# Kernel tuning notes

Measured on AMD Instinct MI355X. Metric: run time of the kernel, lower is better.

The kernel has to match this reference:

```python
import jax, jax.numpy as jnp
import numpy as np

B, L, C = 4, 2048, 1024

def setup_inputs() -> dict:
    key = jax.random.key(0)
    k1, k2, k3 = jax.random.split(key, 3)
    net_in = jax.random.normal(k1, (B, L, C), dtype=jnp.float32)
    # torch Linear weights stored as (out, in); we keep that convention
    w_qkv = jax.random.normal(k2, (3 * C, C), dtype=jnp.float32) * (1.0 / np.sqrt(C))
    w_out = jax.random.normal(k3, (C, C), dtype=jnp.float32) * (1.0 / np.sqrt(C))
    return {"net_in": net_in, "w_qkv": w_qkv, "w_out": w_out}

def reference(net_in, w_qkv, w_out):
    Bc, Lc, Cc = net_in.shape
    qkv = jnp.einsum('blc,dc->bld', net_in, w_qkv)  # (B, L, 3C)
    q, k, v = jnp.split(qkv, 3, axis=-1)
    attn = jnp.einsum('bqc,bkc->bqk', q, k) / jnp.sqrt(jnp.float32(Cc))
    causal = jnp.tril(jnp.ones((Lc, Lc), dtype=bool))
    attn = jnp.where(causal[None, :, :], attn, -jnp.inf)
    attn = jax.nn.softmax(attn, axis=-1)
    out = jnp.einsum('bqk,bkc->bqc', attn, v)
    return jnp.einsum('blc,dc->bld', out, w_out)
```

## Files before the change

kernel.cpp:

```cpp
#include <hip/hip_runtime.h>
#include <hip/hip_bf16.h>
#include <cstdint>
#include <cstddef>

typedef __hip_bfloat16 bf16;
typedef float  floatx4 __attribute__((ext_vector_type(4)));
typedef __bf16 bf16x8  __attribute__((ext_vector_type(8)));

typedef __attribute__((address_space(1))) void as1_void;
typedef __attribute__((address_space(3))) void as3_void;

constexpr int Bn = 4, Ln = 2048, Cn = 1024;

__device__ __forceinline__ void store_one(float* p, float v) { *p = v; }
__device__ __forceinline__ void store_one(bf16*  p, float v) { *p = __float2bfloat16(v); }

#define BAR()    asm volatile("s_barrier" ::: "memory")
#define VMCNT0() asm volatile("s_waitcnt vmcnt(0)" ::: "memory")
#define SCHEDB() __builtin_amdgcn_sched_barrier(0)
#define STAGE(gp, off) \
    __builtin_amdgcn_global_load_lds((const as1_void*)(gp), (as3_void*)(smem + (off)), 16, 0, 0)

template <typename OutT>
__device__ __forceinline__ void gemm128(
    char* __restrict__ smem,
    const bf16* __restrict__ A, const bf16* __restrict__ B, OutT* __restrict__ C,
    int m0, int n0, int kend, int lda, int ldb, int ldc, float cscale)
{
    const int tid  = threadIdx.x;
    const int lane = tid & 63;
    const int quad = lane >> 4;
    const int lr   = lane & 15;
    const int wave = tid >> 6;
    const int wm   = (wave >> 2) * 64;
    const int wn   = (wave & 3) * 32;

    floatx4 acc[4][2];
#pragma unroll
    for (int i = 0; i < 4; ++i)
#pragma unroll
        for (int j = 0; j < 2; ++j) { floatx4 z = {0.f, 0.f, 0.f, 0.f}; acc[i][j] = z; }

    const int srow = tid >> 3;
    const int sx   = (tid & 7) ^ (srow & 7);
    const bf16* gA = A + (size_t)(m0 + srow) * lda + sx * 8;
    const bf16* gB = B + (size_t)(n0 + srow) * ldb + sx * 8;
    const int wuni = __builtin_amdgcn_readfirstlane((tid & 0x1C0) * 16);

    const int aoff = (wm + lr) * 64;
    const int boff = (wn + lr) * 64;
    const int s0   = (quad ^ (lr & 7)) * 8;

    const int NT  = kend >> 6;
    const int BUF = 32768;

#define STG4(KN, bo) do { \
        STAGE(gA + (KN),            (bo) + 0 * 8192 + wuni); \
        STAGE(gA + (KN) + 64 * lda, (bo) + 1 * 8192 + wuni); \
        STAGE(gB + (KN),            (bo) + 16384 + 0 * 8192 + wuni); \
        STAGE(gB + (KN) + 64 * ldb, (bo) + 16384 + 1 * 8192 + wuni); } while (0)

    STG4(0, 0);
    VMCNT0();
    BAR();

#define LDA2(PH, SK) do { _Pragma("unroll") for (int ii = 0; ii < 2; ++ii) \
        a[ii] = *(const bf16x8*)(As + aoff + ((PH) * 2 + ii) * 1024 + (SK)); } while (0)
#define LDB2(SK) do { _Pragma("unroll") for (int nn = 0; nn < 2; ++nn) \
        b[nn] = *(const bf16x8*)(Bs + boff + nn * 1024 + (SK)); } while (0)
#define MFMA4(PH) do { _Pragma("unroll") for (int ii = 0; ii < 2; ++ii) { \
        _Pragma("unroll") for (int nn = 0; nn < 2; ++nn) \
            acc[(PH) * 2 + ii][nn] = __builtin_amdgcn_mfma_f32_16x16x32_bf16( \
                a[ii], b[nn], acc[(PH) * 2 + ii][nn], 0, 0, 0); } } while (0)

    for (int t = 0; t < NT; ++t) {
        const bf16* As = (const bf16*)(smem + (t & 1) * BUF);
        const bf16* Bs = (const bf16*)(smem + (t & 1) * BUF + 16384);
        const int  wl  = ((t + 1) & 1) * BUF;
        const int  kn  = (t + 1) << 6;
        const bool more = (t + 1 < NT);
        bf16x8 a[2], b[2];

        LDB2(s0);
        LDA2(0, s0);
        if (more) STG4(kn, wl);
        BAR(); SCHEDB();
        __builtin_amdgcn_s_setprio(1);
        MFMA4(0);
        __builtin_amdgcn_s_setprio(0);
        SCHEDB();
        BAR();

        LDA2(1, s0);
        BAR(); SCHEDB();
        __builtin_amdgcn_s_setprio(1);
        MFMA4(1);
        __builtin_amdgcn_s_setprio(0);
        SCHEDB();
        BAR();

        LDB2(s0 ^ 32);
        LDA2(0, s0 ^ 32);
        BAR(); SCHEDB();
        __builtin_amdgcn_s_setprio(1);
        MFMA4(0);
        __builtin_amdgcn_s_setprio(0);
        SCHEDB();
        BAR();

        LDA2(1, s0 ^ 32);
        BAR(); SCHEDB();
        __builtin_amdgcn_s_setprio(1);
        MFMA4(1);
        __builtin_amdgcn_s_setprio(0);
        SCHEDB();
        if (more) VMCNT0();
        BAR();
    }
#undef LDA2
#undef LDB2
#undef MFMA4
#undef STG4

#pragma unroll
    for (int mi = 0; mi < 4; ++mi) {
        const int row = m0 + wm + mi * 16 + quad * 4;
#pragma unroll
        for (int n = 0; n < 2; ++n) {
            const int col = n0 + wn + n * 16 + lr;
            OutT* cp = C + (size_t)row * ldc + col;
#pragma unroll
            for (int r = 0; r < 4; ++r)
                store_one(cp + (size_t)r * ldc, acc[mi][n][r] * cscale);
        }
    }
}

__global__ __launch_bounds__(512, 4)
void g1_qk(const bf16* __restrict__ Xb, const bf16* __restrict__ Wqkb,
           bf16* __restrict__ QK)
{
    __shared__ __align__(16) char smem[65536];
    const int i = blockIdx.x;
    const int x = i & 7;
    const int r = i >> 3;
    const int mt = x * 8 + (r & 7);
    const int nt = r >> 3;
    gemm128<bf16>(smem, Xb, Wqkb, QK, mt * 128, nt * 128, 1024, 1024, 1024, 2048, 1.0f);
}

__global__ __launch_bounds__(512, 4)
void g2_s_w2(const bf16* __restrict__ QK, const bf16* __restrict__ Wob,
             const bf16* __restrict__ WvT, bf16* __restrict__ S,
             bf16* __restrict__ W2)
{
    __shared__ __align__(16) char smem[65536];
    const int i = blockIdx.x;
    if (i < 544) {
        const int b = (i & 7) >> 1;
        const int p = i & 1;
        const int t = (i >> 3) * 2 + p;
        int ti = (int)((sqrtf(8.f * t + 1.f) - 1.f) * 0.5f);
        while ((ti + 1) * (ti + 2) / 2 <= t) ++ti;
        while (ti * (ti + 1) / 2 > t) --ti;
        const int tj = t - ti * (ti + 1) / 2;
        const bf16* Aq = QK + (size_t)b * Ln * 2048;
        const bf16* Bk = Aq + 1024;
        bf16* Sb = S + (size_t)b * Ln * Ln;
        gemm128<bf16>(smem, Aq, Bk, Sb, ti * 128, tj * 128, 1024, 2048, 2048, Ln, 0.03125f);
    } else {
        const int j = i - 544;
        gemm128<bf16>(smem, Wob, WvT, W2, (j >> 3) * 128, (j & 7) * 128, 1024, 1024, 1024, 1024, 1.0f);
    }
}

__device__ __forceinline__ float waveMax(float x) {
#pragma unroll
    for (int o = 32; o > 0; o >>= 1) x = fmaxf(x, __shfl_xor(x, o, 64));
    return x;
}
__device__ __forceinline__ float waveSum(float x) {
#pragma unroll
    for (int o = 32; o > 0; o >>= 1) x += __shfl_xor(x, o, 64);
    return x;
}

__device__ void softmax_rows16(bf16* __restrict__ S, int i)
{
    const int wave = threadIdx.x >> 6, lane = threadIdx.x & 63;
    for (int it2 = 0; it2 < 2; ++it2) {
        const int row = i + 512 * (wave * 2 + it2);
        const int q = row & (Ln - 1);
        bf16* Srow = S + (size_t)row * Ln;
        const int kmax = ((q >> 7) + 1) << 7;
        const int nv = (kmax + 511) >> 9;
        float x[4][8];
        float m = -1e30f;
        for (int it = 0; it < nv; ++it) {
            int c0 = it * 512 + lane * 8;
            bf16x8 v = *(const bf16x8*)(Srow + c0);
#pragma unroll
            for (int e = 0; e < 8; ++e) {
                float f = (float)v[e];
                f = (c0 + e <= q) ? f : -1e30f;
                x[it][e] = f;
                m = fmaxf(m, f);
            }
        }
        m = waveMax(m);
        float s = 0.f;
        for (int it = 0; it < nv; ++it)
#pragma unroll
            for (int e = 0; e < 8; ++e) {
                float ex = (x[it][e] > -1e29f) ? __expf(x[it][e] - m) : 0.f;
                x[it][e] = ex;
                s += ex;
            }
        s = waveSum(s);
        const float inv = 1.f / s;
        for (int it = 0; it < nv; ++it) {
            bf16x8 o;
#pragma unroll
            for (int e = 0; e < 8; ++e) o[e] = (__bf16)(x[it][e] * inv);
            *(bf16x8*)(Srow + it * 512 + lane * 8) = o;
        }
    }
}

__global__ __launch_bounds__(512, 4)
void g3_vwt_sm(const bf16* __restrict__ W2, const bf16* __restrict__ Xb,
               bf16* __restrict__ VWT, bf16* __restrict__ S)
{
    __shared__ __align__(16) char smem[65536];
    const int i = blockIdx.x;
    const int x = i & 7;
    const int r = i >> 3;
    const int nt = x * 8 + (r & 7);
    const int mh = r >> 3;
    gemm128<bf16>(smem, W2, Xb, VWT, mh * 128, nt * 128, 1024, 1024, 1024, 8192, 1.0f);
    softmax_rows16(S, i);
}

__global__ __launch_bounds__(512, 4)
void g4_out(const bf16* __restrict__ P, const bf16* __restrict__ VWT,
            float* __restrict__ out)
{
    __shared__ __align__(16) char smem[65536];
    const int i = blockIdx.x;
    const int b = (i & 7) >> 1, p = i & 1;
    const int nt = p * 4 + ((i >> 3) & 3);
    const int mh = 15 - (i >> 5);

    const bf16* Pp = P + (size_t)b * Ln * Ln;
    const bf16* Bv = VWT + (size_t)b * Ln;
    float* Co = out + (size_t)b * Ln * Cn;
    gemm128<float>(smem, Pp, Bv, Co, mh * 128, nt * 128, (mh + 1) * 128, Ln, 8192, Cn, 1.0f);
}

__global__ __launch_bounds__(256)
void cast_all(const float* __restrict__ X, const float* __restrict__ Wqkv,
              const float* __restrict__ Wo,
              bf16* __restrict__ Xb, bf16* __restrict__ Wqkb,
              bf16* __restrict__ Wob, bf16* __restrict__ WvT)
{
    int blk = blockIdx.x;
    if (blk < 11264) {
        int i = blk * 256 + threadIdx.x;
        const float* src; bf16* dst; int off;
        if (i < 2097152)                 { src = X;    dst = Xb;   off = i; }
        else if (i < 2097152 + 524288)   { src = Wqkv; dst = Wqkb; off = i - 2097152; }
        else                             { src = Wo;   dst = Wob;  off = i - 2621440; }
        float4 f = ((const float4*)src)[off];
        bf16 o0 = __float2bfloat16(f.x), o1 = __float2bfloat16(f.y);
        bf16 o2 = __float2bfloat16(f.z), o3 = __float2bfloat16(f.w);
        ushort4 u;
        u.x = *(unsigned short*)&o0; u.y = *(unsigned short*)&o1;
        u.z = *(unsigned short*)&o2; u.w = *(unsigned short*)&o3;
        *(ushort4*)(dst + (size_t)off * 4) = u;
    } else {
        __shared__ float t[32][33];
        int tt = blk - 11264;
        int c0 = (tt & 31) * 32;
        int r0 = (tt >> 5) * 32;
        const float* Wv = Wqkv + 2048 * 1024;
        int xcol = threadIdx.x & 31, y0 = threadIdx.x >> 5;
#pragma unroll
        for (int p = 0; p < 4; ++p) {
            int y = y0 + 8 * p;
            t[y][xcol] = Wv[(size_t)(r0 + y) * 1024 + c0 + xcol];
        }
        __syncthreads();
#pragma unroll
        for (int p = 0; p < 4; ++p) {
            int mloc = y0 + 8 * p;
            WvT[(size_t)(c0 + mloc) * 1024 + r0 + xcol] = __float2bfloat16(t[xcol][mloc]);
        }
    }
}

extern "C" void kernel_launch(void* const* d_in, const int* in_sizes, int n_in,
                              void* d_out, int out_size, void* d_ws, size_t ws_size,
                              hipStream_t stream)
{
    const float* X    = (const float*)d_in[0];
    const float* Wqkv = (const float*)d_in[1];
    const float* Wout = (const float*)d_in[2];
    float* out = (float*)d_out;

    char* ws = (char*)d_ws;
    const size_t MiB = 1024ull * 1024ull;
    bf16* Xb   = (bf16*)(ws + 0);
    bf16* QK   = (bf16*)(ws + 16 * MiB);
    bf16* VWT  = (bf16*)(ws + 48 * MiB);
    bf16* Sbuf = (bf16*)(ws + 64 * MiB);
    bf16* Wqkb = (bf16*)(ws + 96 * MiB);
    bf16* WvT  = (bf16*)(ws + 100 * MiB);
    bf16* Wob  = (bf16*)(ws + 102 * MiB);
    bf16* W2   = (bf16*)(ws + 104 * MiB);

    cast_all<<<dim3(12288), 256, 0, stream>>>(X, Wqkv, Wout, Xb, Wqkb, Wob, WvT);

    g1_qk<<<dim3(1024), 512, 0, stream>>>(Xb, Wqkb, QK);

    g2_s_w2<<<dim3(608), 512, 0, stream>>>(QK, Wob, WvT, Sbuf, W2);

    g3_vwt_sm<<<dim3(512), 512, 0, stream>>>(W2, Xb, VWT, Sbuf);

    g4_out<<<dim3(512), 512, 0, stream>>>(Sbuf, VWT, out);
}
```

Baseline: 228.2 us.

## Use 128x256 single-buffered GEMM tiles and rebalance work across kernels

Adds a 128x256 tile GEMM with a single 48KB LDS buffer and uses it for the QK projection, the Wout·Wv product and the VWT GEMM. The W2 GEMM moves from the S kernel into the QK kernel, and softmax runs in its own blocks instead of after each GEMM block in g3. Larger tiles raise arithmetic intensity and cut block count. In exchange, the single-buffered loop waits on every K-tile load with no overlap, and register pressure rises with a 4x4 accumulator array.

```diff
diff --git a/kernel.cpp b/kernel.cpp
--- a/kernel.cpp
+++ b/kernel.cpp
@@ -20,6 +20,88 @@
 #define SCHEDB() __builtin_amdgcn_sched_barrier(0)
 #define STAGE(gp, off) \
     __builtin_amdgcn_global_load_lds((const as1_void*)(gp), (as3_void*)(smem + (off)), 16, 0, 0)
+
+template <typename OutT>
+__device__ __forceinline__ void gemm_sb_m128n256(
+    char* __restrict__ smem,
+    const bf16* __restrict__ A, const bf16* __restrict__ B, OutT* __restrict__ C,
+    int m0, int n0, int kend, int lda, int ldb, int ldc, float cscale)
+{
+    const int tid  = threadIdx.x;
+    const int lane = tid & 63;
+    const int quad = lane >> 4;
+    const int lr   = lane & 15;
+    const int wave = tid >> 6;
+    const int wm   = (wave >> 2) * 64;
+    const int wn   = (wave & 3) * 64;
+
+    floatx4 acc[4][4];
+#pragma unroll
+    for (int i = 0; i < 4; ++i)
+#pragma unroll
+        for (int j = 0; j < 4; ++j) { floatx4 z = {0.f, 0.f, 0.f, 0.f}; acc[i][j] = z; }
+
+    const int srow = tid >> 3;
+    const int sx   = (tid & 7) ^ (srow & 7);
+    const bf16* gA = A + (size_t)(m0 + srow) * lda + sx * 8;
+    const bf16* gB = B + (size_t)(n0 + srow) * ldb + sx * 8;
+    const int wuni = __builtin_amdgcn_readfirstlane((tid & 0x1C0) * 16);
+
+    const int aoff = (wm + lr) * 64;
+    const int boff = (wn + lr) * 64;
+    const int s0   = (quad ^ (lr & 7)) * 8;
+
+    const int NT = kend >> 6;
+    const bf16* As = (const bf16*)smem;
+    const bf16* Bs = (const bf16*)(smem + 16384);
+
+    for (int t = 0; t < NT; ++t) {
+        const int kn = t << 6;
+        STAGE(gA + kn,             0 * 8192 + wuni);
+        STAGE(gA + kn + 64 * lda,  1 * 8192 + wuni);
+        STAGE(gB + kn,             16384 + 0 * 8192 + wuni);
+        STAGE(gB + kn + 64  * ldb, 16384 + 1 * 8192 + wuni);
+        STAGE(gB + kn + 128 * ldb, 16384 + 2 * 8192 + wuni);
+        STAGE(gB + kn + 192 * ldb, 16384 + 3 * 8192 + wuni);
+        VMCNT0();
+        BAR();
+        SCHEDB();
+#pragma unroll
+        for (int kk = 0; kk < 2; ++kk) {
+            const int sk = s0 ^ (kk << 5);
+            bf16x8 a[4], b[4];
+#pragma unroll
+            for (int ii = 0; ii < 4; ++ii)
+                a[ii] = *(const bf16x8*)(As + aoff + ii * 1024 + sk);
+#pragma unroll
+            for (int nn = 0; nn < 4; ++nn)
+                b[nn] = *(const bf16x8*)(Bs + boff + nn * 1024 + sk);
+            __builtin_amdgcn_s_setprio(1);
+#pragma unroll
+            for (int ii = 0; ii < 4; ++ii)
+#pragma unroll
+                for (int nn = 0; nn < 4; ++nn)
+                    acc[ii][nn] = __builtin_amdgcn_mfma_f32_16x16x32_bf16(
+                        a[ii], b[nn], acc[ii][nn], 0, 0, 0);
+            __builtin_amdgcn_s_setprio(0);
+        }
+        SCHEDB();
+        if (t + 1 < NT) BAR();
+    }
+
+#pragma unroll
+    for (int mi = 0; mi < 4; ++mi) {
+        const int row = m0 + wm + mi * 16 + quad * 4;
+#pragma unroll
+        for (int n = 0; n < 4; ++n) {
+            const int col = n0 + wn + n * 16 + lr;
+            OutT* cp = C + (size_t)row * ldc + col;
+#pragma unroll
+            for (int r = 0; r < 4; ++r)
+                store_one(cp + (size_t)r * ldc, acc[mi][n][r] * cscale);
+        }
+    }
+}
 
 template <typename OutT>
 __device__ __forceinline__ void gemm128(
@@ -138,40 +220,39 @@
 
 __global__ __launch_bounds__(512, 4)
 void g1_qk(const bf16* __restrict__ Xb, const bf16* __restrict__ Wqkb,
-           bf16* __restrict__ QK)
+           const bf16* __restrict__ Wob, const bf16* __restrict__ WvT,
+           bf16* __restrict__ QK, bf16* __restrict__ W2)
+{
+    __shared__ __align__(16) char smem[49152];
+    const int i = blockIdx.x;
+    if (i < 512) {
+        const int x = i & 7;
+        const int r = i >> 3;
+        const int mt = x * 8 + (r & 7);
+        const int nt = r >> 3;
+        gemm_sb_m128n256<bf16>(smem, Xb, Wqkb, QK, mt * 128, nt * 256, 1024, 1024, 1024, 2048, 1.0f);
+    } else {
+        const int j = i - 512;
+        gemm_sb_m128n256<bf16>(smem, Wob, WvT, W2, (j >> 2) * 128, (j & 3) * 256, 1024, 1024, 1024, 1024, 1.0f);
+    }
+}
+
+__global__ __launch_bounds__(512, 4)
+void g2_s(const bf16* __restrict__ QK, bf16* __restrict__ S)
 {
     __shared__ __align__(16) char smem[65536];
     const int i = blockIdx.x;
-    const int x = i & 7;
-    const int r = i >> 3;
-    const int mt = x * 8 + (r & 7);
-    const int nt = r >> 3;
-    gemm128<bf16>(smem, Xb, Wqkb, QK, mt * 128, nt * 128, 1024, 1024, 1024, 2048, 1.0f);
-}
-
-__global__ __launch_bounds__(512, 4)
-void g2_s_w2(const bf16* __restrict__ QK, const bf16* __restrict__ Wob,
-             const bf16* __restrict__ WvT, bf16* __restrict__ S,
-             bf16* __restrict__ W2)
-{
-    __shared__ __align__(16) char smem[65536];
-    const int i = blockIdx.x;
-    if (i < 544) {
-        const int b = (i & 7) >> 1;
-        const int p = i & 1;
-        const int t = (i >> 3) * 2 + p;
-        int ti = (int)((sqrtf(8.f * t + 1.f) - 1.f) * 0.5f);
-        while ((ti + 1) * (ti + 2) / 2 <= t) ++ti;
-        while (ti * (ti + 1) / 2 > t) --ti;
-        const int tj = t - ti * (ti + 1) / 2;
-        const bf16* Aq = QK + (size_t)b * Ln * 2048;
-        const bf16* Bk = Aq + 1024;
-        bf16* Sb = S + (size_t)b * Ln * Ln;
-        gemm128<bf16>(smem, Aq, Bk, Sb, ti * 128, tj * 128, 1024, 2048, 2048, Ln, 0.03125f);
-    } else {
-        const int j = i - 544;
-        gemm128<bf16>(smem, Wob, WvT, W2, (j >> 3) * 128, (j & 7) * 128, 1024, 1024, 1024, 1024, 1.0f);
-    }
+    const int b = (i & 7) >> 1;
+    const int p = i & 1;
+    const int t = (i >> 3) * 2 + p;
+    int ti = (int)((sqrtf(8.f * t + 1.f) - 1.f) * 0.5f);
+    while ((ti + 1) * (ti + 2) / 2 <= t) ++ti;
+    while (ti * (ti + 1) / 2 > t) --ti;
+    const int tj = t - ti * (ti + 1) / 2;
+    const bf16* Aq = QK + (size_t)b * Ln * 2048;
+    const bf16* Bk = Aq + 1024;
+    bf16* Sb = S + (size_t)b * Ln * Ln;
+    gemm128<bf16>(smem, Aq, Bk, Sb, ti * 128, tj * 128, 1024, 2048, 2048, Ln, 0.03125f);
 }
 
 __device__ __forceinline__ float waveMax(float x) {
@@ -185,11 +266,11 @@
     return x;
 }
 
-__device__ void softmax_rows16(bf16* __restrict__ S, int i)
+__device__ void softmax_rows32(bf16* __restrict__ S, int idx)
 {
     const int wave = threadIdx.x >> 6, lane = threadIdx.x & 63;
-    for (int it2 = 0; it2 < 2; ++it2) {
-        const int row = i + 512 * (wave * 2 + it2);
+    for (int it4 = 0; it4 < 4; ++it4) {
+        const int row = idx + 256 * (wave * 4 + it4);
         const int q = row & (Ln - 1);
         bf16* Srow = S + (size_t)row * Ln;
         const int kmax = ((q >> 7) + 1) << 7;
@@ -231,14 +312,17 @@
 void g3_vwt_sm(const bf16* __restrict__ W2, const bf16* __restrict__ Xb,
                bf16* __restrict__ VWT, bf16* __restrict__ S)
 {
-    __shared__ __align__(16) char smem[65536];
+    __shared__ __align__(16) char smem[49152];
     const int i = blockIdx.x;
-    const int x = i & 7;
-    const int r = i >> 3;
-    const int nt = x * 8 + (r & 7);
-    const int mh = r >> 3;
-    gemm128<bf16>(smem, W2, Xb, VWT, mh * 128, nt * 128, 1024, 1024, 1024, 8192, 1.0f);
-    softmax_rows16(S, i);
+    if (i < 256) {
+        const int x = i & 7;
+        const int r = i >> 3;
+        const int nt = x * 4 + (r & 3);
+        const int mh = r >> 2;
+        gemm_sb_m128n256<bf16>(smem, W2, Xb, VWT, mh * 128, nt * 256, 1024, 1024, 1024, 8192, 1.0f);
+    } else {
+        softmax_rows32(S, i - 256);
+    }
 }
 
 __global__ __launch_bounds__(512, 4)
@@ -320,9 +404,9 @@
 
     cast_all<<<dim3(12288), 256, 0, stream>>>(X, Wqkv, Wout, Xb, Wqkb, Wob, WvT);
 
-    g1_qk<<<dim3(1024), 512, 0, stream>>>(Xb, Wqkb, QK);
-
-    g2_s_w2<<<dim3(608), 512, 0, stream>>>(QK, Wob, WvT, Sbuf, W2);
+    g1_qk<<<dim3(544), 512, 0, stream>>>(Xb, Wqkb, Wob, WvT, QK, W2);
+
+    g2_s<<<dim3(544), 512, 0, stream>>>(QK, Sbuf);
 
     g3_vwt_sm<<<dim3(512), 512, 0, stream>>>(W2, Xb, VWT, Sbuf);
 
```

After: 233.4 us. 1.02x slower.

## Rebalance stages: move W2 into QK kernel, VWT into S kernel, standalone softmax, paired out tiles

Applied to the files above, without the earlier changes.

The W2 = Wo·WvT GEMM now runs in the first kernel alongside the QK projection, and the VWT GEMM runs alongside the causal S GEMM, so each launch has more independent work. Softmax becomes its own kernel with 256 blocks handling four rows per wave. The output GEMM pairs a long and a short causal row tile in each block (h and 15-h), giving every block equal work across half as many blocks. The aim is to even out the triangular load imbalance and cut tail effects between stages, at the cost of one extra launch and softmax no longer overlapping with a GEMM.

```diff
diff --git a/kernel.cpp b/kernel.cpp
--- a/kernel.cpp
+++ b/kernel.cpp
@@ -138,21 +138,27 @@
 
 __global__ __launch_bounds__(512, 4)
 void g1_qk(const bf16* __restrict__ Xb, const bf16* __restrict__ Wqkb,
-           bf16* __restrict__ QK)
+           const bf16* __restrict__ Wob, const bf16* __restrict__ WvT,
+           bf16* __restrict__ QK, bf16* __restrict__ W2)
 {
     __shared__ __align__(16) char smem[65536];
     const int i = blockIdx.x;
-    const int x = i & 7;
-    const int r = i >> 3;
-    const int mt = x * 8 + (r & 7);
-    const int nt = r >> 3;
-    gemm128<bf16>(smem, Xb, Wqkb, QK, mt * 128, nt * 128, 1024, 1024, 1024, 2048, 1.0f);
+    if (i < 1024) {
+        const int x = i & 7;
+        const int r = i >> 3;
+        const int mt = x * 8 + (r & 7);
+        const int nt = r >> 3;
+        gemm128<bf16>(smem, Xb, Wqkb, QK, mt * 128, nt * 128, 1024, 1024, 1024, 2048, 1.0f);
+    } else {
+        const int j = i - 1024;
+        gemm128<bf16>(smem, Wob, WvT, W2, (j >> 3) * 128, (j & 7) * 128, 1024, 1024, 1024, 1024, 1.0f);
+    }
 }
 
 __global__ __launch_bounds__(512, 4)
-void g2_s_w2(const bf16* __restrict__ QK, const bf16* __restrict__ Wob,
-             const bf16* __restrict__ WvT, bf16* __restrict__ S,
-             bf16* __restrict__ W2)
+void g2_sv(const bf16* __restrict__ QK, const bf16* __restrict__ W2,
+           const bf16* __restrict__ Xb, bf16* __restrict__ S,
+           bf16* __restrict__ VWT)
 {
     __shared__ __align__(16) char smem[65536];
     const int i = blockIdx.x;
@@ -170,7 +176,11 @@
         gemm128<bf16>(smem, Aq, Bk, Sb, ti * 128, tj * 128, 1024, 2048, 2048, Ln, 0.03125f);
     } else {
         const int j = i - 544;
-        gemm128<bf16>(smem, Wob, WvT, W2, (j >> 3) * 128, (j & 7) * 128, 1024, 1024, 1024, 1024, 1.0f);
+        const int x = j & 7;
+        const int r = j >> 3;
+        const int nt = x * 8 + (r & 7);
+        const int mh = r >> 3;
+        gemm128<bf16>(smem, W2, Xb, VWT, mh * 128, nt * 128, 1024, 1024, 1024, 8192, 1.0f);
     }
 }
 
@@ -185,11 +195,13 @@
     return x;
 }
 
-__device__ void softmax_rows16(bf16* __restrict__ S, int i)
-{
+__global__ __launch_bounds__(512)
+void g3_sm(bf16* __restrict__ S)
+{
+    const int idx = blockIdx.x;
     const int wave = threadIdx.x >> 6, lane = threadIdx.x & 63;
-    for (int it2 = 0; it2 < 2; ++it2) {
-        const int row = i + 512 * (wave * 2 + it2);
+    for (int it4 = 0; it4 < 4; ++it4) {
+        const int row = idx + 256 * (wave * 4 + it4);
         const int q = row & (Ln - 1);
         bf16* Srow = S + (size_t)row * Ln;
         const int kmax = ((q >> 7) + 1) << 7;
@@ -228,20 +240,6 @@
 }
 
 __global__ __launch_bounds__(512, 4)
-void g3_vwt_sm(const bf16* __restrict__ W2, const bf16* __restrict__ Xb,
-               bf16* __restrict__ VWT, bf16* __restrict__ S)
-{
-    __shared__ __align__(16) char smem[65536];
-    const int i = blockIdx.x;
-    const int x = i & 7;
-    const int r = i >> 3;
-    const int nt = x * 8 + (r & 7);
-    const int mh = r >> 3;
-    gemm128<bf16>(smem, W2, Xb, VWT, mh * 128, nt * 128, 1024, 1024, 1024, 8192, 1.0f);
-    softmax_rows16(S, i);
-}
-
-__global__ __launch_bounds__(512, 4)
 void g4_out(const bf16* __restrict__ P, const bf16* __restrict__ VWT,
             float* __restrict__ out)
 {
@@ -249,12 +247,15 @@
     const int i = blockIdx.x;
     const int b = (i & 7) >> 1, p = i & 1;
     const int nt = p * 4 + ((i >> 3) & 3);
-    const int mh = 15 - (i >> 5);
+    const int h = i >> 5;
 
     const bf16* Pp = P + (size_t)b * Ln * Ln;
     const bf16* Bv = VWT + (size_t)b * Ln;
     float* Co = out + (size_t)b * Ln * Cn;
-    gemm128<float>(smem, Pp, Bv, Co, mh * 128, nt * 128, (mh + 1) * 128, Ln, 8192, Cn, 1.0f);
+    const int n0 = nt * 128;
+
+    gemm128<float>(smem, Pp, Bv, Co, (15 - h) * 128, n0, (16 - h) * 128, Ln, 8192, Cn, 1.0f);
+    gemm128<float>(smem, Pp, Bv, Co, h * 128,        n0, (h + 1) * 128,  Ln, 8192, Cn, 1.0f);
 }
 
 __global__ __launch_bounds__(256)
@@ -320,11 +321,11 @@
 
     cast_all<<<dim3(12288), 256, 0, stream>>>(X, Wqkv, Wout, Xb, Wqkb, Wob, WvT);
 
-    g1_qk<<<dim3(1024), 512, 0, stream>>>(Xb, Wqkb, QK);
-
-    g2_s_w2<<<dim3(608), 512, 0, stream>>>(QK, Wob, WvT, Sbuf, W2);
-
-    g3_vwt_sm<<<dim3(512), 512, 0, stream>>>(W2, Xb, VWT, Sbuf);
-
-    g4_out<<<dim3(512), 512, 0, stream>>>(Sbuf, VWT, out);
-}
+    g1_qk<<<dim3(1088), 512, 0, stream>>>(Xb, Wqkb, Wob, WvT, QK, W2);
+
+    g2_sv<<<dim3(1056), 512, 0, stream>>>(QK, W2, Xb, Sbuf, VWT);
+
+    g3_sm<<<dim3(256), 512, 0, stream>>>(Sbuf);
+
+    g4_out<<<dim3(256), 512, 0, stream>>>(Sbuf, VWT, out);
+}
```

Measured after the change: 225.9 us. No clear change (-1.0%).
